# Performance work log

Hardware: AMD Instinct MI355X
Metric: run time of the kernel (lower is better)

The kernel has to match this reference:

```python
import jax, jax.numpy as jnp
import numpy as np

# Pangu-Weather EarthAttention3D, dim=192 branch
H = 6                 # heads
D = 192               # dim
DH = D // H           # head dim = 32
N = 2 * 6 * 12        # window tokens = 144
TW = (8 // 2) * (186 // 6)  # type_of_windows = 124
NW = 8                # number of windows (leading batch axis)
SCALE = DH ** -0.5


def setup_inputs() -> dict:
    key = jax.random.key(0)
    ks = jax.random.split(key, 7)
    return {
        "x": jax.random.normal(ks[0], (NW, TW, N, D), jnp.float32),
        "mask": jax.random.normal(ks[1], (NW, TW, N, N), jnp.float32),
        "w_qkv": jax.random.normal(ks[2], (D, 3 * D), jnp.float32) * 0.02,
        "b_qkv": jnp.zeros((3 * D,), jnp.float32),
        "bias": jax.random.normal(ks[3], (1, TW, H, N, N), jnp.float32) * 0.02,
        "w_out": jax.random.normal(ks[4], (D, D), jnp.float32) * 0.02,
        "b_out": jnp.zeros((D,), jnp.float32),
    }


def reference(x, mask, w_qkv, b_qkv, bias, w_out, b_out):
    B, W, Ntok, Dm = x.shape  # (nW, type_of_windows, win_tokens, dim)
    # fused QKV projection
    qkv = (x @ w_qkv + b_qkv).reshape(B, W, Ntok, 3, H, DH)
    qkv = jnp.transpose(qkv, (3, 0, 1, 4, 2, 5))  # (3, B, W, H, N, dh)
    q, k, v = qkv[0] * SCALE, qkv[1], qkv[2]
    # scores + earth-specific bias + window mask (broadcast over heads)
    attn = jnp.einsum('bwhnd,bwhmd->bwhnm', q, k)
    attn = attn + bias + mask[:, :, None, :, :]
    attn = jax.nn.softmax(attn, axis=-1)  # dropout_rate=0 -> identity
    out = jnp.einsum('bwhnm,bwhmd->bwhnd', attn, v)
    out = jnp.transpose(out, (0, 1, 3, 2, 4)).reshape(B, W, Ntok, Dm)
    return out @ w_out + b_out
```

## Files before the change

kernel.cpp:

```cpp
#include <hip/hip_runtime.h>
#include <hip/hip_bf16.h>

typedef __bf16 bf16_t;
typedef bf16_t bf16x8 __attribute__((ext_vector_type(8)));
typedef bf16_t bf16x4 __attribute__((ext_vector_type(4)));
typedef float f32x4 __attribute__((ext_vector_type(4)));

#define SCALE 0.17677669529663687f

#define PIN(x) asm volatile("" : "+v"(x))

__device__ __forceinline__ int swz_elem(int r, int c) {
    int g = c >> 3;
    return r * 192 + ((g >> 3) << 6) + (((g & 7) ^ (r & 7)) << 3) + (c & 7);
}

__device__ __forceinline__ void stage_chunk(bf16_t* dst, const bf16_t* src, int tid) {
#pragma unroll
    for (int it = 0; it < 3; ++it) {
        int off = (it * 256 + tid) * 8;
        __builtin_amdgcn_global_load_lds(
            (const __attribute__((address_space(1))) unsigned int*)(src + off),
            (__attribute__((address_space(3))) unsigned int*)(dst + off),
            16, 0, 0);
    }
}

__global__ void prep_weights(const float* __restrict__ w_qkv, const float* __restrict__ w_out,
                             bf16_t* __restrict__ wqkvS, bf16_t* __restrict__ woutS) {
    int i = blockIdx.x * 256 + threadIdx.x;
    if (i < 576 * 192) {
        int o = i / 192, k = i % 192;
        float v = w_qkv[k * 576 + o];
        if (o < 192) v *= SCALE;
        wqkvS[(o >> 5) * 6144 + swz_elem(o & 31, k)] = (bf16_t)v;
    }
    if (i < 192 * 192) {
        int o = i / 192, k = i % 192;
        woutS[(o >> 5) * 6144 + swz_elem(o & 31, k)] = (bf16_t)w_out[k * 192 + o];
    }
}

__global__ __launch_bounds__(256, 4)
void qkv_gemm(const float* __restrict__ x, const float* __restrict__ b_qkv,
              const bf16_t* __restrict__ wqkvS,
              bf16_t* __restrict__ Qg, bf16_t* __restrict__ Kg, bf16_t* __restrict__ Vt)
{
    __shared__ __align__(16) bf16_t Wb[2][6144];
    __shared__ __align__(16) bf16_t T[4][1280];
    const int tid  = threadIdx.x;
    const int lane = tid & 63;
    const int wave = tid >> 6;
    const int lrow = lane & 15;
    const int lgrp = lane >> 4;
    const int r0   = blockIdx.x * 128 + wave * 32;

    stage_chunk(&Wb[0][0], wqkvS, tid);

    bf16x8 af[2][6];
#pragma unroll
    for (int tt = 0; tt < 2; ++tt)
#pragma unroll
        for (int ks = 0; ks < 6; ++ks) {
            const float* px = x + (size_t)(r0 + tt * 16 + lrow) * 192 + ks * 32 + lgrp * 8;
            f32x4 lo = *(const f32x4*)px;
            f32x4 hi = *(const f32x4*)(px + 4);
            bf16x8 v;
            v[0] = (bf16_t)lo[0]; v[1] = (bf16_t)lo[1]; v[2] = (bf16_t)lo[2]; v[3] = (bf16_t)lo[3];
            v[4] = (bf16_t)hi[0]; v[5] = (bf16_t)hi[1]; v[6] = (bf16_t)hi[2]; v[7] = (bf16_t)hi[3];
            af[tt][ks] = v;
        }
    __syncthreads();

    bf16_t* tl = &T[wave][0];

    for (int hc = 0; hc < 18; ++hc) {
        if (hc < 17) stage_chunk(&Wb[(hc + 1) & 1][0], wqkvS + (hc + 1) * 6144, tid);
        const bf16_t* wb = &Wb[hc & 1][0];

        f32x4 a[2][2];
        a[0][0] = f32x4{0.f,0.f,0.f,0.f}; a[0][1] = f32x4{0.f,0.f,0.f,0.f};
        a[1][0] = f32x4{0.f,0.f,0.f,0.f}; a[1][1] = f32x4{0.f,0.f,0.f,0.f};
#pragma unroll
        for (int ks = 0; ks < 6; ++ks) {
            bf16x8 wf0 = *(const bf16x8*)&wb[swz_elem(lrow,      ks * 32 + lgrp * 8)];
            bf16x8 wf1 = *(const bf16x8*)&wb[swz_elem(16 + lrow, ks * 32 + lgrp * 8)];
#pragma unroll
            for (int tt = 0; tt < 2; ++tt) {
                a[tt][0] = __builtin_amdgcn_mfma_f32_16x16x32_bf16(af[tt][ks], wf0, a[tt][0], 0, 0, 0);
                a[tt][1] = __builtin_amdgcn_mfma_f32_16x16x32_bf16(af[tt][ks], wf1, a[tt][1], 0, 0, 0);
            }
        }
        __syncthreads();

        float b0 = b_qkv[hc * 32 + lrow], b1 = b_qkv[hc * 32 + 16 + lrow];
        if (hc < 6) { b0 *= SCALE; b1 *= SCALE; }

        if (hc < 12) {
            const int h = (hc < 6) ? hc : hc - 6;
            bf16_t* dst = (hc < 6) ? Qg : Kg;
#pragma unroll
            for (int tt = 0; tt < 2; ++tt) {
#pragma unroll
                for (int j = 0; j < 4; ++j) {
                    tl[tt * 640 + (lgrp * 4 + j) * 40 + lrow]      = (bf16_t)(a[tt][0][j] + b0);
                    tl[tt * 640 + (lgrp * 4 + j) * 40 + 16 + lrow] = (bf16_t)(a[tt][1][j] + b1);
                }
                bf16x8 val = *(const bf16x8*)&tl[tt * 640 + lrow * 40 + lgrp * 8];
                int tk = r0 + tt * 16 + lrow, bw = tk / 144, n = tk % 144;
                *(bf16x8*)&dst[((size_t)(bw * 6 + h) * 144 + n) * 32 + lgrp * 8] = val;
            }
        } else {
            const int hv = hc - 12;
#pragma unroll
            for (int tt = 0; tt < 2; ++tt)
#pragma unroll
                for (int j = 0; j < 4; ++j) {
                    tl[(lrow) * 40      + tt * 16 + lgrp * 4 + j] = (bf16_t)(a[tt][0][j] + b0);
                    tl[(16 + lrow) * 40 + tt * 16 + lgrp * 4 + j] = (bf16_t)(a[tt][1][j] + b1);
                }
#pragma unroll
            for (int it = 0; it < 2; ++it) {
                int slot = it * 64 + lane;
                int d = slot >> 2, c = slot & 3;
                int tk = r0 + c * 8, bw = tk / 144, n = tk % 144;
                bf16x8 val = *(const bf16x8*)&tl[d * 40 + c * 8];
                *(bf16x8*)&Vt[((size_t)(bw * 6 + hv) * 32 + d) * 160 + n] = val;
            }
        }
    }
}

__global__ __launch_bounds__(256, 2)
void earth_attn_v7(const bf16_t* __restrict__ Qg, const bf16_t* __restrict__ Kg,
                   const bf16_t* __restrict__ Vt,
                   const float* __restrict__ mask, const float* __restrict__ bias,
                   bf16_t* __restrict__ Og)
{
    __shared__ bf16_t P[4][16 * 168];
    const int tid  = threadIdx.x;
    const int lane = tid & 63;
    const int wave = tid >> 6;
    const int lrow = lane & 15;
    const int lgrp = lane >> 4;

    const int orig = blockIdx.x;
    const int blk  = (orig & 7) * 186 + (orig >> 3);

    const int wid = blk * 4 + wave;
    const int ww  = wid / 48;
    const int r1  = wid % 48;
    const int b   = r1 / 6;
    const int h   = r1 % 6;
    const int bw  = b * 124 + ww;

    const size_t kbase = ((size_t)(bw * 6 + h) * 144) * 32;
    const size_t vbase = ((size_t)(bw * 6 + h) * 32) * 160;

    bf16x8 ka[9];
#pragma unroll
    for (int nt = 0; nt < 9; ++nt)
        ka[nt] = *(const bf16x8*)&Kg[kbase + (size_t)(nt * 16 + lrow) * 32 + lgrp * 8];

    bf16x8 va0[5], va1[5];
#pragma unroll
    for (int ks = 0; ks < 5; ++ks) {
        va0[ks] = *(const bf16x8*)&Vt[vbase + (size_t)lrow * 160 + ks * 32 + lgrp * 8];
        va1[ks] = *(const bf16x8*)&Vt[vbase + (size_t)(16 + lrow) * 160 + ks * 32 + lgrp * 8];
    }

    const float* bp_base = bias + (size_t)(ww * 6 + h) * 144 * 144;
    const float* mp_base = mask + (size_t)bw * 144 * 144;
    bf16_t* pb = &P[wave][0];
    bf16_t* ogp = Og + ((size_t)bw * 144) * 192 + h * 32 + lgrp * 8;

    bf16x8 qa = *(const bf16x8*)&Qg[kbase + (size_t)lrow * 32 + lgrp * 8];
    f32x4 bv[9], mv[9];
    {
        const float* bp = bp_base + (size_t)lrow * 144;
        const float* mp = mp_base + (size_t)lrow * 144;
#pragma unroll
        for (int nt = 0; nt < 9; ++nt) {
            bv[nt] = *(const f32x4*)(bp + nt * 16 + lgrp * 4);
            mv[nt] = *(const f32x4*)(mp + nt * 16 + lgrp * 4);
        }
    }

#pragma unroll 1
    for (int t = 0; t < 9; ++t) {
        f32x4 s[9];
#pragma unroll
        for (int nt = 0; nt < 9; ++nt) s[nt] = bv[nt] + mv[nt];

        const int tn = (t < 8) ? t + 1 : 8;
        bf16x8 qa_n = *(const bf16x8*)&Qg[kbase + (size_t)(tn * 16 + lrow) * 32 + lgrp * 8];
        PIN(qa_n);
        {
            const float* bp = bp_base + (size_t)(tn * 16 + lrow) * 144;
            const float* mp = mp_base + (size_t)(tn * 16 + lrow) * 144;
#pragma unroll
            for (int nt = 0; nt < 9; ++nt) {
                bv[nt] = *(const f32x4*)(bp + nt * 16 + lgrp * 4);
                mv[nt] = *(const f32x4*)(mp + nt * 16 + lgrp * 4);
            }
#pragma unroll
            for (int nt = 0; nt < 9; ++nt) { PIN(bv[nt]); PIN(mv[nt]); }
        }

#pragma unroll
        for (int nt = 0; nt < 9; ++nt)
            s[nt] = __builtin_amdgcn_mfma_f32_16x16x32_bf16(ka[nt], qa, s[nt], 0, 0, 0);

        float mx = -1e30f;
#pragma unroll
        for (int nt = 0; nt < 9; ++nt)
#pragma unroll
            for (int j = 0; j < 4; ++j) mx = fmaxf(mx, s[nt][j]);
        mx = fmaxf(mx, __shfl_xor(mx, 16, 64));
        mx = fmaxf(mx, __shfl_xor(mx, 32, 64));
        float sum = 0.f;
#pragma unroll
        for (int nt = 0; nt < 9; ++nt)
#pragma unroll
            for (int j = 0; j < 4; ++j) { float e = __expf(s[nt][j] - mx); s[nt][j] = e; sum += e; }
        sum += __shfl_xor(sum, 16, 64);
        sum += __shfl_xor(sum, 32, 64);
        const float rinv = 1.0f / sum;

#pragma unroll
        for (int nt = 0; nt < 9; ++nt) {
            bf16x4 pw;
#pragma unroll
            for (int j = 0; j < 4; ++j) pw[j] = (bf16_t)(s[nt][j] * rinv);
            *(bf16x4*)&pb[lrow * 168 + nt * 16 + lgrp * 4] = pw;
        }
        {
            uint2 z2 = make_uint2(0u, 0u);
            *(uint2*)&pb[lrow * 168 + 144 + lgrp * 4] = z2;
        }

        bf16x8 pa[5];
#pragma unroll
        for (int ks = 0; ks < 5; ++ks)
            pa[ks] = *(const bf16x8*)&pb[lrow * 168 + ks * 32 + lgrp * 8];
#pragma unroll
        for (int ks = 0; ks < 5; ++ks) PIN(pa[ks]);

        f32x4 o0{0.f, 0.f, 0.f, 0.f}, o1{0.f, 0.f, 0.f, 0.f};
#pragma unroll
        for (int ks = 0; ks < 5; ++ks) {
            o0 = __builtin_amdgcn_mfma_f32_16x16x32_bf16(pa[ks], va0[ks], o0, 0, 0, 0);
            o1 = __builtin_amdgcn_mfma_f32_16x16x32_bf16(pa[ks], va1[ks], o1, 0, 0, 0);
        }

#pragma unroll
        for (int j = 0; j < 4; ++j) {
            pb[(lgrp * 4 + j) * 168 + lrow]      = (bf16_t)o0[j];
            pb[(lgrp * 4 + j) * 168 + 16 + lrow] = (bf16_t)o1[j];
        }
        bf16x8 ov = *(const bf16x8*)&pb[lrow * 168 + lgrp * 8];
        *(bf16x8*)(ogp + (size_t)(t * 16 + lrow) * 192) = ov;

        qa = qa_n;
    }
}

__global__ __launch_bounds__(256, 4)
void out_proj(const bf16_t* __restrict__ Og, const bf16_t* __restrict__ woutS,
              const float* __restrict__ b_out, float* __restrict__ out)
{
    __shared__ __align__(16) bf16_t Wb[2][6144];
    const int tid  = threadIdx.x;
    const int lane = tid & 63;
    const int wave = tid >> 6;
    const int lrow = lane & 15;
    const int lgrp = lane >> 4;
    const size_t row0 = (size_t)blockIdx.x * 64 + wave * 16;

    stage_chunk(&Wb[0][0], woutS, tid);

    bf16x8 af[6];
#pragma unroll
    for (int ks = 0; ks < 6; ++ks)
        af[ks] = *(const bf16x8*)(Og + (row0 + lrow) * 192 + ks * 32 + lgrp * 8);
    __syncthreads();

#pragma unroll
    for (int c = 0; c < 6; ++c) {
        if (c < 5) stage_chunk(&Wb[(c + 1) & 1][0], woutS + (c + 1) * 6144, tid);
        const bf16_t* wb = &Wb[c & 1][0];
        float b0 = b_out[c * 32 + lrow], b1 = b_out[c * 32 + 16 + lrow];
        f32x4 a0{b0, b0, b0, b0}, a1{b1, b1, b1, b1};
#pragma unroll
        for (int ks = 0; ks < 6; ++ks) {
            bf16x8 wf0 = *(const bf16x8*)&wb[swz_elem(lrow,      ks * 32 + lgrp * 8)];
            bf16x8 wf1 = *(const bf16x8*)&wb[swz_elem(16 + lrow, ks * 32 + lgrp * 8)];
            a0 = __builtin_amdgcn_mfma_f32_16x16x32_bf16(af[ks], wf0, a0, 0, 0, 0);
            a1 = __builtin_amdgcn_mfma_f32_16x16x32_bf16(af[ks], wf1, a1, 0, 0, 0);
        }
        __syncthreads();
#pragma unroll
        for (int j = 0; j < 4; ++j) {
            out[(row0 + lgrp * 4 + j) * 192 + c * 32 + lrow]      = a0[j];
            out[(row0 + lgrp * 4 + j) * 192 + c * 32 + 16 + lrow] = a1[j];
        }
    }
}

extern "C" void kernel_launch(void* const* d_in, const int* in_sizes, int n_in,
                              void* d_out, int out_size, void* d_ws, size_t ws_size,
                              hipStream_t stream) {
    const float* x     = (const float*)d_in[0];
    const float* mask  = (const float*)d_in[1];
    const float* w_qkv = (const float*)d_in[2];
    const float* b_qkv = (const float*)d_in[3];
    const float* bias  = (const float*)d_in[4];
    const float* w_out = (const float*)d_in[5];
    const float* b_out = (const float*)d_in[6];

    bf16_t* wqkvS = (bf16_t*)d_ws;
    bf16_t* woutS = wqkvS + 576 * 192;
    bf16_t* Qg    = woutS + 192 * 192;
    bf16_t* Kg    = Qg + (size_t)992 * 6 * 144 * 32;
    bf16_t* Vt    = Kg + (size_t)992 * 6 * 144 * 32;
    bf16_t* Og    = Vt + (size_t)992 * 6 * 32 * 160;

    prep_weights<<<dim3(432), dim3(256), 0, stream>>>(w_qkv, w_out, wqkvS, woutS);
    qkv_gemm<<<dim3(1116), dim3(256), 0, stream>>>(x, b_qkv, wqkvS, Qg, Kg, Vt);
    earth_attn_v7<<<dim3(1488), dim3(256), 0, stream>>>(Qg, Kg, Vt, mask, bias, Og);
    out_proj<<<dim3(2232), dim3(256), 0, stream>>>(Og, woutS, b_out, (float*)d_out);
}
```

Baseline: 263.6 us.

## Pre-convert bias and mask to bf16 fragment layout before attention

```diff
diff --git a/kernel.cpp b/kernel.cpp
--- a/kernel.cpp
+++ b/kernel.cpp
@@ -38,6 +38,37 @@
     if (i < 192 * 192) {
         int o = i / 192, k = i % 192;
         woutS[(o >> 5) * 6144 + swz_elem(o & 31, k)] = (bf16_t)w_out[k * 192 + o];
+    }
+}
+
+__global__ __launch_bounds__(256)
+void prep_bm(const float* __restrict__ bias, const float* __restrict__ mask,
+             bf16_t* __restrict__ biasP, bf16_t* __restrict__ maskP)
+{
+    int gid = blockIdx.x * 256 + threadIdx.x;
+    const int NB = 6696 * 64;
+    const int NM = 8928 * 64;
+    bool isMask = gid >= NB;
+    if (isMask) gid -= NB;
+    if (isMask && gid >= NM) return;
+    const int lane = gid & 63;
+    const int region = gid >> 6;
+    const int lrow = lane & 15, lgrp = lane >> 4;
+    const int t = region % 9, rg = region / 9;
+    const float* src = (isMask ? mask : bias) + ((size_t)rg * 144 + t * 16 + lrow) * 144 + lgrp * 4;
+    bf16_t* dst = (isMask ? maskP : biasP) + (size_t)region * 2560 + lane * 8;
+#pragma unroll
+    for (int it = 0; it < 5; ++it) {
+        f32x4 v0 = *(const f32x4*)(src + it * 32);
+        bf16x8 o;
+        o[0] = (bf16_t)v0[0]; o[1] = (bf16_t)v0[1]; o[2] = (bf16_t)v0[2]; o[3] = (bf16_t)v0[3];
+        if (it < 4) {
+            f32x4 v1 = *(const f32x4*)(src + it * 32 + 16);
+            o[4] = (bf16_t)v1[0]; o[5] = (bf16_t)v1[1]; o[6] = (bf16_t)v1[2]; o[7] = (bf16_t)v1[3];
+        } else {
+            o[4] = o[5] = o[6] = o[7] = (bf16_t)0.f;
+        }
+        *(bf16x8*)(dst + it * 512) = o;
     }
 }
 
@@ -132,6 +163,137 @@
 }
 
 __global__ __launch_bounds__(256, 2)
+void earth_attn_v8(const bf16_t* __restrict__ Qg, const bf16_t* __restrict__ Kg,
+                   const bf16_t* __restrict__ Vt,
+                   const bf16_t* __restrict__ maskP, const bf16_t* __restrict__ biasP,
+                   bf16_t* __restrict__ Og)
+{
+    __shared__ bf16_t P[4][16 * 168];
+    const int tid  = threadIdx.x;
+    const int lane = tid & 63;
+    const int wave = tid >> 6;
+    const int lrow = lane & 15;
+    const int lgrp = lane >> 4;
+
+    const int orig = blockIdx.x;
+    const int blk  = (orig & 7) * 186 + (orig >> 3);
+
+    const int wid = blk * 4 + wave;
+    const int ww  = wid / 48;
+    const int r1  = wid % 48;
+    const int b   = r1 / 6;
+    const int h   = r1 % 6;
+    const int bw  = b * 124 + ww;
+
+    const size_t kbase = ((size_t)(bw * 6 + h) * 144) * 32;
+    const size_t vbase = ((size_t)(bw * 6 + h) * 32) * 160;
+
+    bf16x8 ka[9];
+#pragma unroll
+    for (int nt = 0; nt < 9; ++nt)
+        ka[nt] = *(const bf16x8*)&Kg[kbase + (size_t)(nt * 16 + lrow) * 32 + lgrp * 8];
+
+    bf16x8 va0[5], va1[5];
+#pragma unroll
+    for (int ks = 0; ks < 5; ++ks) {
+        va0[ks] = *(const bf16x8*)&Vt[vbase + (size_t)lrow * 160 + ks * 32 + lgrp * 8];
+        va1[ks] = *(const bf16x8*)&Vt[vbase + (size_t)(16 + lrow) * 160 + ks * 32 + lgrp * 8];
+    }
+
+    const bf16_t* bpB = biasP + (size_t)(ww * 6 + h) * 9 * 2560 + lane * 8;
+    const bf16_t* mpB = maskP + (size_t)bw * 9 * 2560 + lane * 8;
+    bf16_t* pb = &P[wave][0];
+    bf16_t* ogp = Og + ((size_t)bw * 144) * 192 + h * 32 + lgrp * 8;
+
+    bf16x8 qa = *(const bf16x8*)&Qg[kbase + (size_t)lrow * 32 + lgrp * 8];
+    bf16x8 bvv[5], mvv[5];
+#pragma unroll
+    for (int it = 0; it < 5; ++it) {
+        bvv[it] = *(const bf16x8*)(bpB + it * 512);
+        mvv[it] = *(const bf16x8*)(mpB + it * 512);
+    }
+
+#pragma unroll 1
+    for (int t = 0; t < 9; ++t) {
+        f32x4 s[9];
+#pragma unroll
+        for (int nt = 0; nt < 9; ++nt)
+#pragma unroll
+            for (int j = 0; j < 4; ++j) {
+                const int u = nt * 4 + j;
+                s[nt][j] = (float)bvv[u >> 3][u & 7] + (float)mvv[u >> 3][u & 7];
+            }
+
+        const int tn = (t < 8) ? t + 1 : 8;
+        bf16x8 qa_n = *(const bf16x8*)&Qg[kbase + (size_t)(tn * 16 + lrow) * 32 + lgrp * 8];
+        PIN(qa_n);
+#pragma unroll
+        for (int it = 0; it < 5; ++it) {
+            bvv[it] = *(const bf16x8*)(bpB + (size_t)tn * 2560 + it * 512);
+            mvv[it] = *(const bf16x8*)(mpB + (size_t)tn * 2560 + it * 512);
+        }
+#pragma unroll
+        for (int it = 0; it < 5; ++it) { PIN(bvv[it]); PIN(mvv[it]); }
+
+#pragma unroll
+        for (int nt = 0; nt < 9; ++nt)
+            s[nt] = __builtin_amdgcn_mfma_f32_16x16x32_bf16(ka[nt], qa, s[nt], 0, 0, 0);
+
+        float mx = -1e30f;
+#pragma unroll
+        for (int nt = 0; nt < 9; ++nt)
+#pragma unroll
+            for (int j = 0; j < 4; ++j) mx = fmaxf(mx, s[nt][j]);
+        mx = fmaxf(mx, __shfl_xor(mx, 16, 64));
+        mx = fmaxf(mx, __shfl_xor(mx, 32, 64));
+        float sum = 0.f;
+#pragma unroll
+        for (int nt = 0; nt < 9; ++nt)
+#pragma unroll
+            for (int j = 0; j < 4; ++j) { float e = __expf(s[nt][j] - mx); s[nt][j] = e; sum += e; }
+        sum += __shfl_xor(sum, 16, 64);
+        sum += __shfl_xor(sum, 32, 64);
+        const float rinv = 1.0f / sum;
+
+#pragma unroll
+        for (int nt = 0; nt < 9; ++nt) {
+            bf16x4 pw;
+#pragma unroll
+            for (int j = 0; j < 4; ++j) pw[j] = (bf16_t)(s[nt][j] * rinv);
+            *(bf16x4*)&pb[lrow * 168 + nt * 16 + lgrp * 4] = pw;
+        }
+        {
+            uint2 z2 = make_uint2(0u, 0u);
+            *(uint2*)&pb[lrow * 168 + 144 + lgrp * 4] = z2;
+        }
+
+        bf16x8 pa[5];
+#pragma unroll
+        for (int ks = 0; ks < 5; ++ks)
+            pa[ks] = *(const bf16x8*)&pb[lrow * 168 + ks * 32 + lgrp * 8];
+#pragma unroll
+        for (int ks = 0; ks < 5; ++ks) PIN(pa[ks]);
+
+        f32x4 o0{0.f, 0.f, 0.f, 0.f}, o1{0.f, 0.f, 0.f, 0.f};
+#pragma unroll
+        for (int ks = 0; ks < 5; ++ks) {
+            o0 = __builtin_amdgcn_mfma_f32_16x16x32_bf16(pa[ks], va0[ks], o0, 0, 0, 0);
+            o1 = __builtin_amdgcn_mfma_f32_16x16x32_bf16(pa[ks], va1[ks], o1, 0, 0, 0);
+        }
+
+#pragma unroll
+        for (int j = 0; j < 4; ++j) {
+            pb[(lgrp * 4 + j) * 168 + lrow]      = (bf16_t)o0[j];
+            pb[(lgrp * 4 + j) * 168 + 16 + lrow] = (bf16_t)o1[j];
+        }
+        bf16x8 ov = *(const bf16x8*)&pb[lrow * 168 + lgrp * 8];
+        *(bf16x8*)(ogp + (size_t)(t * 16 + lrow) * 192) = ov;
+
+        qa = qa_n;
+    }
+}
+
+__global__ __launch_bounds__(256, 2)
 void earth_attn_v7(const bf16_t* __restrict__ Qg, const bf16_t* __restrict__ Kg,
                    const bf16_t* __restrict__ Vt,
                    const float* __restrict__ mask, const float* __restrict__ bias,
@@ -143,17 +305,14 @@
     const int wave = tid >> 6;
     const int lrow = lane & 15;
     const int lgrp = lane >> 4;
-
     const int orig = blockIdx.x;
     const int blk  = (orig & 7) * 186 + (orig >> 3);
-
     const int wid = blk * 4 + wave;
     const int ww  = wid / 48;
     const int r1  = wid % 48;
     const int b   = r1 / 6;
     const int h   = r1 % 6;
     const int bw  = b * 124 + ww;
-
     const size_t kbase = ((size_t)(bw * 6 + h) * 144) * 32;
     const size_t vbase = ((size_t)(bw * 6 + h) * 32) * 160;
 
@@ -161,19 +320,16 @@
 #pragma unroll
     for (int nt = 0; nt < 9; ++nt)
         ka[nt] = *(const bf16x8*)&Kg[kbase + (size_t)(nt * 16 + lrow) * 32 + lgrp * 8];
-
     bf16x8 va0[5], va1[5];
 #pragma unroll
     for (int ks = 0; ks < 5; ++ks) {
         va0[ks] = *(const bf16x8*)&Vt[vbase + (size_t)lrow * 160 + ks * 32 + lgrp * 8];
         va1[ks] = *(const bf16x8*)&Vt[vbase + (size_t)(16 + lrow) * 160 + ks * 32 + lgrp * 8];
     }
-
     const float* bp_base = bias + (size_t)(ww * 6 + h) * 144 * 144;
     const float* mp_base = mask + (size_t)bw * 144 * 144;
     bf16_t* pb = &P[wave][0];
     bf16_t* ogp = Og + ((size_t)bw * 144) * 192 + h * 32 + lgrp * 8;
-
     bf16x8 qa = *(const bf16x8*)&Qg[kbase + (size_t)lrow * 32 + lgrp * 8];
     f32x4 bv[9], mv[9];
     {
@@ -185,13 +341,11 @@
             mv[nt] = *(const f32x4*)(mp + nt * 16 + lgrp * 4);
         }
     }
-
 #pragma unroll 1
     for (int t = 0; t < 9; ++t) {
         f32x4 s[9];
 #pragma unroll
         for (int nt = 0; nt < 9; ++nt) s[nt] = bv[nt] + mv[nt];
-
         const int tn = (t < 8) ? t + 1 : 8;
         bf16x8 qa_n = *(const bf16x8*)&Qg[kbase + (size_t)(tn * 16 + lrow) * 32 + lgrp * 8];
         PIN(qa_n);
@@ -206,11 +360,9 @@
 #pragma unroll
             for (int nt = 0; nt < 9; ++nt) { PIN(bv[nt]); PIN(mv[nt]); }
         }
-
 #pragma unroll
         for (int nt = 0; nt < 9; ++nt)
             s[nt] = __builtin_amdgcn_mfma_f32_16x16x32_bf16(ka[nt], qa, s[nt], 0, 0, 0);
-
         float mx = -1e30f;
 #pragma unroll
         for (int nt = 0; nt < 9; ++nt)
@@ -226,7 +378,6 @@
         sum += __shfl_xor(sum, 16, 64);
         sum += __shfl_xor(sum, 32, 64);
         const float rinv = 1.0f / sum;
-
 #pragma unroll
         for (int nt = 0; nt < 9; ++nt) {
             bf16x4 pw;
@@ -238,21 +389,18 @@
             uint2 z2 = make_uint2(0u, 0u);
             *(uint2*)&pb[lrow * 168 + 144 + lgrp * 4] = z2;
         }
-
         bf16x8 pa[5];
 #pragma unroll
         for (int ks = 0; ks < 5; ++ks)
             pa[ks] = *(const bf16x8*)&pb[lrow * 168 + ks * 32 + lgrp * 8];
 #pragma unroll
         for (int ks = 0; ks < 5; ++ks) PIN(pa[ks]);
-
         f32x4 o0{0.f, 0.f, 0.f, 0.f}, o1{0.f, 0.f, 0.f, 0.f};
 #pragma unroll
         for (int ks = 0; ks < 5; ++ks) {
             o0 = __builtin_amdgcn_mfma_f32_16x16x32_bf16(pa[ks], va0[ks], o0, 0, 0, 0);
             o1 = __builtin_amdgcn_mfma_f32_16x16x32_bf16(pa[ks], va1[ks], o1, 0, 0, 0);
         }
-
 #pragma unroll
         for (int j = 0; j < 4; ++j) {
             pb[(lgrp * 4 + j) * 168 + lrow]      = (bf16_t)o0[j];
@@ -260,7 +408,6 @@
         }
         bf16x8 ov = *(const bf16x8*)&pb[lrow * 168 + lgrp * 8];
         *(bf16x8*)(ogp + (size_t)(t * 16 + lrow) * 192) = ov;
-
         qa = qa_n;
     }
 }
@@ -324,9 +471,19 @@
     bf16_t* Kg    = Qg + (size_t)992 * 6 * 144 * 32;
     bf16_t* Vt    = Kg + (size_t)992 * 6 * 144 * 32;
     bf16_t* Og    = Vt + (size_t)992 * 6 * 32 * 160;
+    bf16_t* biasP = Og + (size_t)992 * 144 * 192;
+    bf16_t* maskP = biasP + (size_t)6696 * 2560;
+
+    const size_t need_v8 = ((size_t)112902144 + 17141760 + 22855680) * 2;
 
     prep_weights<<<dim3(432), dim3(256), 0, stream>>>(w_qkv, w_out, wqkvS, woutS);
     qkv_gemm<<<dim3(1116), dim3(256), 0, stream>>>(x, b_qkv, wqkvS, Qg, Kg, Vt);
-    earth_attn_v7<<<dim3(1488), dim3(256), 0, stream>>>(Qg, Kg, Vt, mask, bias, Og);
+
+    if (ws_size >= need_v8) {
+        prep_bm<<<dim3(3906), dim3(256), 0, stream>>>(bias, mask, biasP, maskP);
+        earth_attn_v8<<<dim3(1488), dim3(256), 0, stream>>>(Qg, Kg, Vt, maskP, biasP, Og);
+    } else {
+        earth_attn_v7<<<dim3(1488), dim3(256), 0, stream>>>(Qg, Kg, Vt, mask, bias, Og);
+    }
     out_proj<<<dim3(2232), dim3(256), 0, stream>>>(Og, woutS, b_out, (float*)d_out);
 }
```

Result: slower. 285.1 us (+8.2%).
